# Performance work log

Hardware: AMD Instinct MI355X
Metric: run time of the kernel (lower is better)

The kernel has to match this reference:

```python
import jax, jax.numpy as jnp
import numpy as np

N_NODES = 50000
N_EDGES = 800000
IN_DIM = 128
OUT_DIM = 64


def setup_inputs() -> dict:
    key = jax.random.key(0)
    k_x, k_r, k_c, k_v, k_w = jax.random.split(key, 5)
    x = jax.random.normal(k_x, (N_NODES, IN_DIM), dtype=jnp.float32)
    edge_row = jax.random.randint(k_r, (N_EDGES,), 0, N_NODES, dtype=jnp.int64)
    edge_col = jax.random.randint(k_c, (N_EDGES,), 0, N_NODES, dtype=jnp.int64)
    edge_val = jax.random.uniform(k_v, (N_EDGES,), dtype=jnp.float32)
    # kaiming_uniform-style init: bound = sqrt(6 / fan_in) with a=sqrt(5) gain folded in torch;
    # exact init values don't affect correctness testing, use a uniform of similar scale.
    bound = float(np.sqrt(6.0 / IN_DIM))
    weight = jax.random.uniform(k_w, (IN_DIM, OUT_DIM), dtype=jnp.float32,
                                minval=-bound, maxval=bound)
    return {"x": x, "edge_row": edge_row, "edge_col": edge_col,
            "edge_val": edge_val, "weight": weight}


def reference(x, edge_row, edge_col, edge_val, weight):
    # dropout p=0.0 -> identity (module default)
    support = x @ weight                              # [N, out_dim] dense GEMM
    # spmm(adj, support): out[i] = sum_e adj_val[e] * support[col[e]] for row[e]==i
    messages = edge_val[:, None] * support[edge_col]  # [E, out_dim] gather
    out = jax.ops.segment_sum(messages, edge_row, num_segments=N_NODES)  # scatter-add
    return jax.nn.relu(out)
```

## Files before the change

kernel.cpp:

```cpp
#include <hip/hip_runtime.h>

#define N_NODES 50000
#define N_EDGES 800000
#define IN_DIM 128
#define OUT_DIM 64

#define GROUP_SHIFT 6
#define GROUP_ROWS 64
#define N_GROUPS 782
#define SLAB 1216
#define CHUNK2 2048
#define FILL3_BLOCKS 391

typedef _Float16 h4 __attribute__((ext_vector_type(4)));
typedef _Float16 h8 __attribute__((ext_vector_type(8)));
typedef float    f4 __attribute__((ext_vector_type(4)));

#define LDK 136

__global__ __launch_bounds__(256) void gemm_mfma(const float* __restrict__ x,
                                                 const float* __restrict__ w,
                                                 _Float16* __restrict__ support) {
    __shared__ _Float16 xb[GROUP_ROWS * LDK];
    __shared__ _Float16 wt[OUT_DIM * LDK];
    const int tid = threadIdx.x;

    for (int i = tid; i < IN_DIM * OUT_DIM; i += 256) {
        int k = i >> 6, n = i & 63;
        wt[n * LDK + k] = (_Float16)w[i];
    }
    const int rowbase = blockIdx.x * GROUP_ROWS;
    for (int i = tid; i < GROUP_ROWS * (IN_DIM / 4); i += 256) {
        int r  = i >> 5;
        int kq = i & 31;
        int row = rowbase + r;
        float4 v = (row < N_NODES) ? *(const float4*)&x[(size_t)row * IN_DIM + kq * 4]
                                   : make_float4(0.f, 0.f, 0.f, 0.f);
        h4 hv = { (_Float16)v.x, (_Float16)v.y, (_Float16)v.z, (_Float16)v.w };
        *(h4*)&xb[r * LDK + kq * 4] = hv;
    }
    __syncthreads();

    const int wave = tid >> 6;
    const int lane = tid & 63;
    const int mrow = lane & 15;
    const int quad = lane >> 4;
    const int m0   = wave * 16;

    f4 acc[4];
    #pragma unroll
    for (int t = 0; t < 4; ++t) acc[t] = (f4){0.f, 0.f, 0.f, 0.f};

    #pragma unroll
    for (int ks = 0; ks < 4; ++ks) {
        int kof = ks * 32 + quad * 8;
        h8 a = *(h8*)&xb[(m0 + mrow) * LDK + kof];
        #pragma unroll
        for (int t = 0; t < 4; ++t) {
            h8 b = *(h8*)&wt[(t * 16 + mrow) * LDK + kof];
            acc[t] = __builtin_amdgcn_mfma_f32_16x16x32_f16(a, b, acc[t], 0, 0, 0);
        }
    }

    #pragma unroll
    for (int t = 0; t < 4; ++t) {
        #pragma unroll
        for (int r = 0; r < 4; ++r) {
            int row = rowbase + m0 + quad * 4 + r;
            if (row < N_NODES)
                support[(size_t)row * OUT_DIM + t * 16 + mrow] = (_Float16)acc[t][r];
        }
    }
}

__global__ __launch_bounds__(256) void fill3_kernel(const int* __restrict__ erow,
                                                    const int* __restrict__ ecol,
                                                    const float* __restrict__ eval,
                                                    int* __restrict__ gcursor,
                                                    int2* __restrict__ bucket) {
    __shared__ int lcnt[N_GROUPS];
    __shared__ int lbase[N_GROUPS];
    for (int i = threadIdx.x; i < N_GROUPS; i += 256) lcnt[i] = 0;
    __syncthreads();
    const int base = blockIdx.x * CHUNK2;
    #pragma unroll 4
    for (int i = 0; i < CHUNK2 / 256; ++i) {
        int e = base + threadIdx.x + i * 256;
        if (e < N_EDGES) atomicAdd(&lcnt[erow[e] >> GROUP_SHIFT], 1);
    }
    __syncthreads();
    for (int i = threadIdx.x; i < N_GROUPS; i += 256) {
        int c = lcnt[i];
        lbase[i] = c ? atomicAdd(&gcursor[i], c) : 0;
        lcnt[i]  = 0;
    }
    __syncthreads();
    #pragma unroll 4
    for (int i = 0; i < CHUNK2 / 256; ++i) {
        int e = base + threadIdx.x + i * 256;
        if (e < N_EDGES) {
            int r = erow[e];
            int g = r >> GROUP_SHIFT;
            int p = atomicAdd(&lcnt[g], 1);
            bucket[(size_t)g * SLAB + lbase[g] + p] =
                make_int2(((r & (GROUP_ROWS - 1)) << 16) | ecol[e],
                          __float_as_int(eval[e]));
        }
    }
}

__global__ __launch_bounds__(256) void sort3_kernel(const int* __restrict__ gcursor,
                                                    int2* __restrict__ bucket,
                                                    int2* __restrict__ offs_cnt) {
    __shared__ int2 ebuf[SLAB];
    __shared__ int  rcnt[GROUP_ROWS];
    __shared__ int  rbase_s[GROUP_ROWS];
    const int grp   = blockIdx.x;
    const int cnt   = gcursor[grp];
    const long long start = (long long)grp * SLAB;
    const int tid   = threadIdx.x;

    if (tid < GROUP_ROWS) rcnt[tid] = 0;
    __syncthreads();
    for (int j = tid; j < cnt; j += 256) {
        int2 cv = bucket[start + j];
        ebuf[j] = cv;
        atomicAdd(&rcnt[cv.x >> 16], 1);
    }
    __syncthreads();
    if (tid < GROUP_ROWS) {
        int v = rcnt[tid];
        int s = v;
        #pragma unroll
        for (int off = 1; off < 64; off <<= 1) {
            int t = __shfl_up(s, off, 64);
            if (tid >= off) s += t;
        }
        int excl = s - v;
        rbase_s[tid] = excl;
        int row = grp * GROUP_ROWS + tid;
        if (row < N_NODES) offs_cnt[row] = make_int2((int)start + excl, v);
        rcnt[tid] = 0;
    }
    __syncthreads();
    for (int j = tid; j < cnt; j += 256) {
        int2 cv = ebuf[j];
        int rl = cv.x >> 16;
        int p  = atomicAdd(&rcnt[rl], 1);
        bucket[start + rbase_s[rl] + p] = cv;
    }
}

__global__ __launch_bounds__(256) void reduce_kernel(const int2* __restrict__ offs_cnt,
                                                     const int2* __restrict__ bucket,
                                                     const _Float16* __restrict__ support,
                                                     float* __restrict__ out) {
    const int g     = threadIdx.x & 15;
    const int local = threadIdx.x >> 4;
    const int row   = blockIdx.x * 16 + local;
    if (row >= N_NODES) return;
    const int2 oc   = offs_cnt[row];
    const int start = oc.x;
    const int end   = oc.x + oc.y;
    float4 acc = make_float4(0.f, 0.f, 0.f, 0.f);
    for (int j = start; j < end; ++j) {
        int2 cv = bucket[j];
        int col = cv.x & 0xFFFF;
        float v = __int_as_float(cv.y);
        h4 sr = *(const h4*)&support[(size_t)col * OUT_DIM + g * 4];
        acc.x += v * (float)sr[0];
        acc.y += v * (float)sr[1];
        acc.z += v * (float)sr[2];
        acc.w += v * (float)sr[3];
    }
    acc.x = fmaxf(acc.x, 0.f);
    acc.y = fmaxf(acc.y, 0.f);
    acc.z = fmaxf(acc.z, 0.f);
    acc.w = fmaxf(acc.w, 0.f);
    *(float4*)&out[(size_t)row * OUT_DIM + g * 4] = acc;
}

extern "C" void kernel_launch(void* const* d_in, const int* in_sizes, int n_in,
                              void* d_out, int out_size, void* d_ws, size_t ws_size,
                              hipStream_t stream) {
    const float* x    = (const float*)d_in[0];
    const int*   erow = (const int*)  d_in[1];
    const int*   ecol = (const int*)  d_in[2];
    const float* ev   = (const float*)d_in[3];
    const float* w    = (const float*)d_in[4];
    float* out = (float*)d_out;

    char* ws = (char*)d_ws;
    _Float16* support = (_Float16*)ws;
    int*  gcursor  = (int*)(ws + 6400000);
    int2* offs_cnt = (int2*)(ws + 6403200);
    int2* bucket   = (int2*)(ws + 6803200);

    hipMemsetAsync(gcursor, 0, sizeof(int) * N_GROUPS, stream);

    gemm_mfma<<<N_GROUPS, 256, 0, stream>>>(x, w, support);
    fill3_kernel<<<FILL3_BLOCKS, 256, 0, stream>>>(erow, ecol, ev, gcursor, bucket);
    sort3_kernel<<<N_GROUPS, 256, 0, stream>>>(gcursor, bucket, offs_cnt);
    reduce_kernel<<<(N_NODES + 15) / 16, 256, 0, stream>>>(offs_cnt, bucket, support, out);
}
```

Measured before the change: 150.3 us.

## Fuse per-group sort with row reduction and drop the cursor memset

```diff
diff --git a/kernel.cpp b/kernel.cpp
--- a/kernel.cpp
+++ b/kernel.cpp
@@ -20,10 +20,13 @@
 
 __global__ __launch_bounds__(256) void gemm_mfma(const float* __restrict__ x,
                                                  const float* __restrict__ w,
-                                                 _Float16* __restrict__ support) {
+                                                 _Float16* __restrict__ support,
+                                                 int* __restrict__ gcursor) {
     __shared__ _Float16 xb[GROUP_ROWS * LDK];
     __shared__ _Float16 wt[OUT_DIM * LDK];
     const int tid = threadIdx.x;
+
+    if (tid == 0) gcursor[blockIdx.x] = 0;
 
     for (int i = tid; i < IN_DIM * OUT_DIM; i += 256) {
         int k = i >> 6, n = i & 63;
@@ -109,16 +112,19 @@
     }
 }
 
-__global__ __launch_bounds__(256) void sort3_kernel(const int* __restrict__ gcursor,
-                                                    int2* __restrict__ bucket,
-                                                    int2* __restrict__ offs_cnt) {
+__global__ __launch_bounds__(256) void group_reduce(const int* __restrict__ gcursor,
+                                                    const int2* __restrict__ bucket,
+                                                    const _Float16* __restrict__ support,
+                                                    float* __restrict__ out) {
     __shared__ int2 ebuf[SLAB];
+    __shared__ int2 ebuf2[SLAB];
     __shared__ int  rcnt[GROUP_ROWS];
-    __shared__ int  rbase_s[GROUP_ROWS];
-    const int grp   = blockIdx.x;
-    const int cnt   = gcursor[grp];
+    __shared__ int  rstart[GROUP_ROWS + 1];
+    __shared__ int  rcur[GROUP_ROWS];
+    const int grp = blockIdx.x;
+    const int cnt = gcursor[grp];
     const long long start = (long long)grp * SLAB;
-    const int tid   = threadIdx.x;
+    const int tid = threadIdx.x;
 
     if (tid < GROUP_ROWS) rcnt[tid] = 0;
     __syncthreads();
@@ -137,47 +143,47 @@
             if (tid >= off) s += t;
         }
         int excl = s - v;
-        rbase_s[tid] = excl;
-        int row = grp * GROUP_ROWS + tid;
-        if (row < N_NODES) offs_cnt[row] = make_int2((int)start + excl, v);
-        rcnt[tid] = 0;
+        rstart[tid] = excl;
+        rcur[tid]   = excl;
+        if (tid == 63) rstart[64] = s;
     }
     __syncthreads();
     for (int j = tid; j < cnt; j += 256) {
         int2 cv = ebuf[j];
         int rl = cv.x >> 16;
-        int p  = atomicAdd(&rcnt[rl], 1);
-        bucket[start + rbase_s[rl] + p] = cv;
-    }
-}
-
-__global__ __launch_bounds__(256) void reduce_kernel(const int2* __restrict__ offs_cnt,
-                                                     const int2* __restrict__ bucket,
-                                                     const _Float16* __restrict__ support,
-                                                     float* __restrict__ out) {
-    const int g     = threadIdx.x & 15;
-    const int local = threadIdx.x >> 4;
-    const int row   = blockIdx.x * 16 + local;
-    if (row >= N_NODES) return;
-    const int2 oc   = offs_cnt[row];
-    const int start = oc.x;
-    const int end   = oc.x + oc.y;
-    float4 acc = make_float4(0.f, 0.f, 0.f, 0.f);
-    for (int j = start; j < end; ++j) {
-        int2 cv = bucket[j];
-        int col = cv.x & 0xFFFF;
-        float v = __int_as_float(cv.y);
-        h4 sr = *(const h4*)&support[(size_t)col * OUT_DIM + g * 4];
-        acc.x += v * (float)sr[0];
-        acc.y += v * (float)sr[1];
-        acc.z += v * (float)sr[2];
-        acc.w += v * (float)sr[3];
-    }
-    acc.x = fmaxf(acc.x, 0.f);
-    acc.y = fmaxf(acc.y, 0.f);
-    acc.z = fmaxf(acc.z, 0.f);
-    acc.w = fmaxf(acc.w, 0.f);
-    *(float4*)&out[(size_t)row * OUT_DIM + g * 4] = acc;
+        int p  = atomicAdd(&rcur[rl], 1);
+        ebuf2[p] = cv;
+    }
+    __syncthreads();
+
+    const int g     = tid & 15;
+    const int local = tid >> 4;
+    const int rowbase = grp * GROUP_ROWS;
+    #pragma unroll
+    for (int rr = 0; rr < 4; ++rr) {
+        const int rl  = local + rr * 16;
+        const int row = rowbase + rl;
+        const int jb  = rstart[rl];
+        const int je  = rstart[rl + 1];
+        float4 acc = make_float4(0.f, 0.f, 0.f, 0.f);
+        for (int j = jb; j < je; ++j) {
+            int2 cv = ebuf2[j];
+            int col = cv.x & 0xFFFF;
+            float v = __int_as_float(cv.y);
+            h4 sr = *(const h4*)&support[(size_t)col * OUT_DIM + g * 4];
+            acc.x += v * (float)sr[0];
+            acc.y += v * (float)sr[1];
+            acc.z += v * (float)sr[2];
+            acc.w += v * (float)sr[3];
+        }
+        if (row < N_NODES) {
+            acc.x = fmaxf(acc.x, 0.f);
+            acc.y = fmaxf(acc.y, 0.f);
+            acc.z = fmaxf(acc.z, 0.f);
+            acc.w = fmaxf(acc.w, 0.f);
+            *(float4*)&out[(size_t)row * OUT_DIM + g * 4] = acc;
+        }
+    }
 }
 
 extern "C" void kernel_launch(void* const* d_in, const int* in_sizes, int n_in,
@@ -192,14 +198,10 @@
 
     char* ws = (char*)d_ws;
     _Float16* support = (_Float16*)ws;
-    int*  gcursor  = (int*)(ws + 6400000);
-    int2* offs_cnt = (int2*)(ws + 6403200);
-    int2* bucket   = (int2*)(ws + 6803200);
-
-    hipMemsetAsync(gcursor, 0, sizeof(int) * N_GROUPS, stream);
-
-    gemm_mfma<<<N_GROUPS, 256, 0, stream>>>(x, w, support);
+    int*  gcursor = (int*)(ws + 6400000);
+    int2* bucket  = (int2*)(ws + 6403200);
+
+    gemm_mfma<<<N_GROUPS, 256, 0, stream>>>(x, w, support, gcursor);
     fill3_kernel<<<FILL3_BLOCKS, 256, 0, stream>>>(erow, ecol, ev, gcursor, bucket);
-    sort3_kernel<<<N_GROUPS, 256, 0, stream>>>(gcursor, bucket, offs_cnt);
-    reduce_kernel<<<(N_NODES + 15) / 16, 256, 0, stream>>>(offs_cnt, bucket, support, out);
-}
+    group_reduce<<<N_GROUPS, 256, 0, stream>>>(gcursor, bucket, support, out);
+}
```

After: 146.1 us. -2.8%, faster.
